# Optimization experiments

Measured on AMD Instinct MI355X. Metric: run time of the kernel, lower is better.

## Reference

```python
import jax, jax.numpy as jnp
import numpy as np

EPS = 1e-5
K = 9  # 3x3 kernel taps


def _deform_conv_bn_relu(x, w_off, b_off, w, gamma, beta):
    B, C, H, W = x.shape
    dt = x.dtype
    # offset-predicting conv: [B, 2*K, H, W], channel layout (y,x) pairs per tap (mmcv v1)
    offset = jax.lax.conv_general_dilated(
        x, w_off, window_strides=(1, 1), padding=((1, 1), (1, 1)),
        dimension_numbers=('NCHW', 'OIHW', 'NCHW')) + b_off[None, :, None, None]
    off = offset.reshape(B, K, 2, H, W)
    # kernel tap displacements relative to output pixel (padding=1 -> centered 3x3)
    dy = (jnp.arange(K) // 3 - 1).astype(dt)
    dx = (jnp.arange(K) % 3 - 1).astype(dt)
    ii = jnp.arange(H, dtype=dt)[:, None]
    jj = jnp.arange(W, dtype=dt)[None, :]
    py = ii[None, None] + dy[None, :, None, None] + off[:, :, 0]  # [B,K,H,W]
    px = jj[None, None] + dx[None, :, None, None] + off[:, :, 1]
    y0 = jnp.floor(py)
    x0 = jnp.floor(px)
    ly = py - y0
    lx = px - x0

    xf = x.reshape(B, C, H * W)

    def gather(yc, xc, wt):
        # bilinear corner gather with zero padding outside the image
        valid = (yc >= 0) & (yc < H) & (xc >= 0) & (xc < W)
        yi = jnp.clip(yc, 0, H - 1).astype(jnp.int32)
        xi = jnp.clip(xc, 0, W - 1).astype(jnp.int32)
        idx = (yi * W + xi).reshape(B, -1)              # [B, K*H*W]
        g = jax.vmap(lambda xb, ib: xb[:, ib])(xf, idx)  # [B, C, K*H*W]
        wm = (wt * valid.astype(dt)).reshape(B, 1, -1)
        return g * wm

    val = (gather(y0, x0, (1 - ly) * (1 - lx))
           + gather(y0, x0 + 1, (1 - ly) * lx)
           + gather(y0 + 1, x0, ly * (1 - lx))
           + gather(y0 + 1, x0 + 1, ly * lx))
    val = val.reshape(B, C, K, H, W)

    # deformable conv accumulation (no bias in mmcv DeformConv2d v1)
    O = w.shape[0]
    out = jnp.einsum('ock,bckhw->bohw', w.reshape(O, C, K), val)

    # BatchNorm (training-mode batch stats) + ReLU
    mean = out.mean(axis=(0, 2, 3))
    var = out.var(axis=(0, 2, 3))
    out = (out - mean[None, :, None, None]) * jax.lax.rsqrt(var + EPS)[None, :, None, None]
    out = out * gamma[None, :, None, None] + beta[None, :, None, None]
    return jax.nn.relu(out)


def setup_inputs() -> dict:
    key = jax.random.key(0)
    k1, k2, k3 = jax.random.split(key, 3)
    B, C, O, H, W = 2, 256, 256, 128, 128
    x = jax.random.normal(k1, (B, C, H, W), dtype=jnp.float32)
    # offset branch: small init so predicted offsets stay in a realistic range
    w_off = jax.random.normal(k2, (2 * K, C, 3, 3), dtype=jnp.float32) * 0.01
    b_off = jnp.zeros((2 * K,), dtype=jnp.float32)
    w = jax.random.normal(k3, (O, C, 3, 3), dtype=jnp.float32) * 0.05
    gamma = jnp.ones((O,), dtype=jnp.float32)
    beta = jnp.zeros((O,), dtype=jnp.float32)
    return {"x": x, "w_off": w_off, "b_off": b_off, "w": w, "gamma": gamma, "beta": beta}


def reference(x, w_off, b_off, w, gamma, beta):
    return _deform_conv_bn_relu(x, w_off, b_off, w, gamma, beta)
```

## Files before the change

### kernel.cpp

```cpp
#include <hip/hip_runtime.h>
#include <hip/hip_bf16.h>

#define HWs   16384
#define Wimg  128
#define Himg  128
#define PW    130
#define PHW   16900
#define Cin   256
#define Oout  256
#define CKd   2304
#define Bb    2

typedef short   bf16x8 __attribute__((ext_vector_type(8)));
typedef float   f32x4  __attribute__((ext_vector_type(4)));

__device__ __forceinline__ float bf2f(ushort u){
  union { unsigned int i; float f; } v; v.i = ((unsigned int)u) << 16; return v.f;
}
__device__ __forceinline__ ushort f2bf(float f){
  union { float f; unsigned int i; } v; v.f = f;
  return (ushort)((v.i + 0x8000u) >> 16);
}
__device__ __forceinline__ unsigned cvt_pk_bf16(float lo, float hi){
  unsigned r;
  asm("v_cvt_pk_bf16_f32 %0, %1, %2" : "=v"(r) : "v"(lo), "v"(hi));
  return r;
}
__device__ __forceinline__ void gload_lds16(const ushort* g, void* l){
  __builtin_amdgcn_global_load_lds(
      (const __attribute__((address_space(1))) unsigned int*)g,
      (__attribute__((address_space(3))) unsigned int*)l, 16, 0, 0);
}

__global__ __launch_bounds__(256) void k_transpose(const float* __restrict__ x,
                                                   ushort* __restrict__ xtp){
  int bx = blockIdx.x;
  int b  = bx >> 10;
  int r  = bx & 1023;
  int ct = r >> 8;
  int pt = r & 255;
  int c0 = ct * 64, p0 = pt * 64;
  __shared__ float tile[64][65];
  const float* xb = x + (size_t)b * Cin * HWs;
  #pragma unroll
  for (int pass = 0; pass < 16; ++pass){
    int idx = pass * 256 + threadIdx.x;
    int cl = idx >> 6, pl = idx & 63;
    tile[cl][pl] = xb[(size_t)(c0 + cl) * HWs + p0 + pl];
  }
  __syncthreads();
  ushort* xo = xtp + (size_t)b * PHW * Cin;
  #pragma unroll
  for (int pass = 0; pass < 16; ++pass){
    int idx = pass * 256 + threadIdx.x;
    int pl = idx >> 6, cl = idx & 63;
    int hw = p0 + pl; int y = hw >> 7, xc = hw & 127;
    xo[(size_t)((y + 1) * PW + xc + 1) * Cin + c0 + cl] = f2bf(tile[cl][pl]);
  }
}

__global__ __launch_bounds__(64) void k_border(ushort* __restrict__ xtp){
  int e = blockIdx.x;
  int b = e / 516, p = e % 516;
  int y, xc;
  if (p < 130)      { y = 0;       xc = p; }
  else if (p < 260) { y = 129;     xc = p - 130; }
  else if (p < 388) { y = p - 259; xc = 0; }
  else              { y = p - 387; xc = 129; }
  uint2* dst = (uint2*)(xtp + ((size_t)b * PHW + y * PW + xc) * Cin) + threadIdx.x;
  *dst = make_uint2(0u, 0u);
}

__global__ __launch_bounds__(256) void k_wprep(const float* __restrict__ w,
                                               const float* __restrict__ wof,
                                               ushort* __restrict__ w2,
                                               ushort* __restrict__ w2of){
  int idx = blockIdx.x * 256 + threadIdx.x;
  if (idx < Oout * CKd){
    int o = idx / CKd, r = idx % CKd;
    int k = r >> 8, c = r & 255;
    w2[idx] = f2bf(w[(size_t)(o * Cin + c) * 9 + k]);
  } else {
    int j = idx - Oout * CKd;
    int o = j / CKd, r = j % CKd;
    int k = r >> 8, c = r & 255;
    float v = (o < 18) ? wof[(size_t)(o * Cin + c) * 9 + k] : 0.f;
    w2of[j] = f2bf(v);
  }
}

__global__ __launch_bounds__(512, 4) void k_offconv(const ushort* __restrict__ xtp,
                                                    const ushort* __restrict__ w2of,
                                                    const float* __restrict__ b_off,
                                                    int4* __restrict__ pidx,
                                                    float4* __restrict__ pw){
  int bx = blockIdx.x;
  int blkm = ((bx & 7) << 6) | (bx >> 3);
  int b = blkm >> 8, tile = blkm & 255;
  int hw0 = tile * 64;
  int iy = tile >> 1, jx0 = (tile & 1) * 64;
  __shared__ __align__(16) ushort aw[2][2048];
  __shared__ __align__(16) ushort bv_s[2][4096];
  __shared__ float offs_lds[18][64];
  int t = threadIdx.x, lane = t & 63, wid = t >> 6;
  int mi = wid >> 2, ni = wid & 3;
  f32x4 acc = (f32x4){0,0,0,0};
  const ushort* xb = xtp + (size_t)b * PHW * Cin;

#define OSTAGE(S, P) \
  if ((S) < 36){ int kks = (S) * 64, kt = (S) >> 2, c0s = ((S) * 64) & 255; \
    int dy = kt / 3 - 1, dxx = kt % 3 - 1; \
    if (wid < 4){ int L = t * 16; int oo = L >> 7; int inb = (L & 127) ^ ((oo & 7) << 4); \
      gload_lds16(w2of + (size_t)oo * CKd + kks + (inb >> 1), (char*)aw[P] + L); } \
    { int L = t * 16; int hw_l = L >> 7; int inb = (L & 127) ^ ((hw_l & 7) << 4); \
      int row = (iy + dy + 1) * PW + (jx0 + hw_l + dxx + 1); \
      gload_lds16(xb + (size_t)row * Cin + c0s + (inb >> 1), (char*)bv_s[P] + L); } }

  OSTAGE(0, 0);
  __syncthreads();
  #pragma unroll 1
  for (int step = 0; step < 36; ++step){
    int P = step & 1;
    OSTAGE(step + 1, P ^ 1);
    #pragma unroll
    for (int kk2 = 0; kk2 < 2; ++kk2){
      int coff = kk2 * 64 + ((lane >> 4) << 4);
      bf16x8 a0, bb;
      { int r = mi * 16 + (lane & 15); int byte = r * 128 + coff; byte ^= ((r & 7) << 4); a0 = *(const bf16x8*)((char*)aw[P] + byte); }
      { int r = ni * 16 + (lane & 15); int byte = r * 128 + coff; byte ^= ((r & 7) << 4); bb = *(const bf16x8*)((char*)bv_s[P] + byte); }
      acc = __builtin_amdgcn_mfma_f32_16x16x32_bf16(a0, bb, acc, 0, 0, 0);
    }
    __syncthreads();
  }
#undef OSTAGE
  {
    int hw_l = ni * 16 + (lane & 15);
    #pragma unroll
    for (int r = 0; r < 4; ++r){
      int o = mi * 16 + ((lane >> 4) << 2) + r;
      if (o < 18) offs_lds[o][hw_l] = acc[r] + b_off[o];
    }
  }
  __syncthreads();
  for (int idx = t; idx < 9 * 64; idx += 512){
    int k = idx >> 6, jl = idx & 63;
    int hw = hw0 + jl;
    int i = hw >> 7, jcol = hw & 127;
    float offy = offs_lds[2 * k][jl];
    float offx = offs_lds[2 * k + 1][jl];
    float py = (float)i    + (float)(k / 3 - 1) + offy;
    float px = (float)jcol + (float)(k % 3 - 1) + offx;
    float y0f = floorf(py), x0f = floorf(px);
    float ly = py - y0f, lx = px - x0f;
    int y0 = (int)y0f, x0 = (int)x0f;
    int y1 = y0 + 1, x1 = x0 + 1;
    float w00 = (1.f - ly) * (1.f - lx), w01 = (1.f - ly) * lx;
    float w10 = ly * (1.f - lx),         w11 = ly * lx;
    bool vy0 = (y0 >= 0 && y0 < 128), vy1 = (y1 >= 0 && y1 < 128);
    bool vx0 = (x0 >= 0 && x0 < 128), vx1 = (x1 >= 0 && x1 < 128);
    int iy0 = min(max(y0, 0), 127), iy1 = min(max(y1, 0), 127);
    int ix0 = min(max(x0, 0), 127), ix1 = min(max(x1, 0), 127);
    size_t e = ((size_t)b * 9 + k) * HWs + hw;
    pidx[e] = make_int4(((iy0 + 1) * PW + ix0 + 1) * Cin, ((iy0 + 1) * PW + ix1 + 1) * Cin,
                        ((iy1 + 1) * PW + ix0 + 1) * Cin, ((iy1 + 1) * PW + ix1 + 1) * Cin);
    pw[e]   = make_float4(vy0 && vx0 ? w00 : 0.f, vy0 && vx1 ? w01 : 0.f,
                          vy1 && vx0 ? w10 : 0.f, vy1 && vx1 ? w11 : 0.f);
  }
}

__device__ __forceinline__ unsigned combine_pair(unsigned d0, unsigned d1, unsigned d2, unsigned d3,
                                                 float4 wt){
  float e0 = wt.x * __uint_as_float(d0 << 16)
           + wt.y * __uint_as_float(d1 << 16)
           + wt.z * __uint_as_float(d2 << 16)
           + wt.w * __uint_as_float(d3 << 16);
  float e1 = wt.x * __uint_as_float(d0 & 0xFFFF0000u)
           + wt.y * __uint_as_float(d1 & 0xFFFF0000u)
           + wt.z * __uint_as_float(d2 & 0xFFFF0000u)
           + wt.w * __uint_as_float(d3 & 0xFFFF0000u);
  return cvt_pk_bf16(e0, e1);
}

__global__ __launch_bounds__(512, 2) void k_main(const ushort* __restrict__ xtp,
                                                 const ushort* __restrict__ w2,
                                                 const int4* __restrict__ pidx,
                                                 const float4* __restrict__ pw,
                                                 float* __restrict__ out,
                                                 float* __restrict__ partials){
  int bx = blockIdx.x;
  int blkm = ((bx & 7) << 5) | (bx >> 3);
  int b = blkm >> 7, tile = blkm & 127;
  int hw0 = tile * 128;
  __shared__ __align__(16) ushort smem[49152];
  ushort* Ab0 = smem;
  ushort* Ab1 = smem + 16384;
  ushort* Bb0 = smem + 32768;
  ushort* Bb1 = smem + 40960;
  int t = threadIdx.x, lane = t & 63, wid = t >> 6;
  int wm = wid >> 1, wn = wid & 1;
  int cg = t & 7, hl = t >> 3;
  f32x4 acc[4][4];
  #pragma unroll
  for (int mi = 0; mi < 4; ++mi)
    #pragma unroll
    for (int ni = 0; ni < 4; ++ni) acc[mi][ni] = (f32x4){0,0,0,0};
  const ushort* xb  = xtp  + (size_t)b * PHW * Cin;
  const int4*   pib = pidx + (size_t)b * 9 * HWs + hw0;
  const float4* pwb = pw   + (size_t)b * 9 * HWs + hw0;

  int4   ids[2][2];
  float4 wts[2][2];
  uint4  g[2][2][4];

#define PIPE_BARRIER() do { \
    asm volatile("s_waitcnt vmcnt(12) lgkmcnt(0)" ::: "memory"); \
    __builtin_amdgcn_sched_barrier(0); \
    __builtin_amdgcn_s_barrier(); \
    __builtin_amdgcn_sched_barrier(0); \
  } while (0)

#define IDSLOAD(P, S) \
  { int kq = ((S) < 35 ? (S) : 35) >> 2; \
    ids[P][0] = pib[(size_t)kq * HWs + hl]; \
    ids[P][1] = pib[(size_t)kq * HWs + hl + 64]; }

#define CORNERS(P, S) \
  { int Sc = ((S) < 35 ? (S) : 35); \
    int cb = ((Sc * 64) & 255) + cg * 8; int kq = Sc >> 2; \
    wts[P][0] = pwb[(size_t)kq * HWs + hl]; \
    wts[P][1] = pwb[(size_t)kq * HWs + hl + 64]; \
    _Pragma("unroll") for (int hh = 0; hh < 2; ++hh){ \
      g[P][hh][0] = *(const uint4*)(xb + ids[P][hh].x + cb); \
      g[P][hh][1] = *(const uint4*)(xb + ids[P][hh].y + cb); \
      g[P][hh][2] = *(const uint4*)(xb + ids[P][hh].z + cb); \
      g[P][hh][3] = *(const uint4*)(xb + ids[P][hh].w + cb); } }

#define STAGEA(S, ABP) \
  { int kks = ((S) < 35 ? (S) : 35) * 64; \
    _Pragma("unroll") for (int h2 = 0; h2 < 4; ++h2){ \
      int L = (wid * 4 + h2) * 1024 + lane * 16; \
      int oo = L >> 7; int inb = (L & 127) ^ ((oo & 7) << 4); \
      gload_lds16(w2 + (size_t)oo * CKd + kks + (inb >> 1), (char*)(ABP) + L); } }

#define COMBINE(P, S, BBP) \
  { _Pragma("unroll") for (int hh = 0; hh < 2; ++hh){ \
      int hw_l = hl + hh * 64; \
      float4 wtv = wts[P][hh]; \
      uint4 ov; \
      ov.x = combine_pair(g[P][hh][0].x, g[P][hh][1].x, g[P][hh][2].x, g[P][hh][3].x, wtv); \
      ov.y = combine_pair(g[P][hh][0].y, g[P][hh][1].y, g[P][hh][2].y, g[P][hh][3].y, wtv); \
      ov.z = combine_pair(g[P][hh][0].z, g[P][hh][1].z, g[P][hh][2].z, g[P][hh][3].z, wtv); \
      ov.w = combine_pair(g[P][hh][0].w, g[P][hh][1].w, g[P][hh][2].w, g[P][hh][3].w, wtv); \
      int byte = hw_l * 128 + cg * 16; byte ^= ((hw_l & 7) << 4); \
      *(uint4*)((char*)(BBP) + byte) = ov; } }

#define MFMA_PHASE(ABP, BBP) \
  { __builtin_amdgcn_s_setprio(1); \
    _Pragma("unroll") for (int kk2 = 0; kk2 < 2; ++kk2){ \
      int coff = kk2 * 64 + ((lane >> 4) << 4); \
      bf16x8 a[4], bv[4]; \
      _Pragma("unroll") for (int mi = 0; mi < 4; ++mi){ \
        int r = wm * 64 + mi * 16 + (lane & 15); \
        int byte = r * 128 + coff; byte ^= ((r & 7) << 4); \
        a[mi] = *(const bf16x8*)((const char*)(ABP) + byte); } \
      _Pragma("unroll") for (int ni = 0; ni < 4; ++ni){ \
        int r = wn * 64 + ni * 16 + (lane & 15); \
        int byte = r * 128 + coff; byte ^= ((r & 7) << 4); \
        bv[ni] = *(const bf16x8*)((const char*)(BBP) + byte); } \
      _Pragma("unroll") for (int mi = 0; mi < 4; ++mi) \
        _Pragma("unroll") for (int ni = 0; ni < 4; ++ni) \
          acc[mi][ni] = __builtin_amdgcn_mfma_f32_16x16x32_bf16(a[mi], bv[ni], acc[mi][ni], 0, 0, 0); } \
    __builtin_amdgcn_s_setprio(0); }

  STAGEA(0, Ab0);
  IDSLOAD(0, 0);
  IDSLOAD(1, 1);
  CORNERS(0, 0);
  IDSLOAD(0, 2);
  CORNERS(1, 1);
  IDSLOAD(1, 3);
  COMBINE(0, 0, Bb0);
  PIPE_BARRIER();

  #pragma unroll 1
  for (int tt = 0; tt < 36; tt += 2){
    STAGEA(tt + 1, Ab1);
    CORNERS(0, tt + 2);
    IDSLOAD(0, tt + 4);
    MFMA_PHASE(Ab0, Bb0);
    COMBINE(1, tt + 1, Bb1);
    PIPE_BARRIER();
    STAGEA(tt + 2, Ab0);
    CORNERS(1, tt + 3);
    IDSLOAD(1, tt + 5);
    MFMA_PHASE(Ab1, Bb1);
    COMBINE(0, tt + 2, Bb0);
    PIPE_BARRIER();
  }
#undef PIPE_BARRIER
#undef IDSLOAD
#undef CORNERS
#undef STAGEA
#undef COMBINE
#undef MFMA_PHASE

  #pragma unroll
  for (int mi = 0; mi < 4; ++mi){
    int obase = wm * 64 + mi * 16 + ((lane >> 4) << 2);
    #pragma unroll
    for (int ni = 0; ni < 4; ++ni){
      int hw = hw0 + wn * 64 + ni * 16 + (lane & 15);
      float* op = out + ((size_t)b * Oout + obase) * HWs + hw;
      #pragma unroll
      for (int r = 0; r < 4; ++r) op[(size_t)r * HWs] = acc[mi][ni][r];
    }
  }
  #pragma unroll
  for (int mi = 0; mi < 4; ++mi){
    #pragma unroll
    for (int r = 0; r < 4; ++r){
      float s = 0.f, s2 = 0.f;
      #pragma unroll
      for (int ni = 0; ni < 4; ++ni){ float v = acc[mi][ni][r]; s += v; s2 += v * v; }
      #pragma unroll
      for (int off2 = 1; off2 < 16; off2 <<= 1){
        s  += __shfl_xor(s, off2);
        s2 += __shfl_xor(s2, off2);
      }
      if ((lane & 15) == 0){
        int o = wm * 64 + mi * 16 + ((lane >> 4) << 2) + r;
        int row = blkm * 2 + wn;
        partials[(size_t)row * 256 + o] = s;
        partials[(size_t)512 * 256 + (size_t)row * 256 + o] = s2;
      }
    }
  }
}

__global__ __launch_bounds__(256) void k_bnstats(const float* __restrict__ partials,
                                                 float* __restrict__ stats){
  int o = blockIdx.x, t = threadIdx.x;
  float s = 0.f, s2 = 0.f;
  for (int i = t; i < 512; i += 256){
    s  += partials[(size_t)i * 256 + o];
    s2 += partials[(size_t)512 * 256 + (size_t)i * 256 + o];
  }
  #pragma unroll
  for (int off = 32; off > 0; off >>= 1){
    s  += __shfl_down(s, off);
    s2 += __shfl_down(s2, off);
  }
  __shared__ float rs[4], rs2[4];
  int lane = t & 63, w = t >> 6;
  if (lane == 0){ rs[w] = s; rs2[w] = s2; }
  __syncthreads();
  if (t == 0){
    float S = 0.f, S2 = 0.f;
    for (int i = 0; i < 4; ++i){ S += rs[i]; S2 += rs2[i]; }
    float mean = S / 32768.f;
    float var  = S2 / 32768.f - mean * mean;
    stats[o] = mean;
    stats[256 + o] = rsqrtf(var + 1e-5f);
  }
}

__global__ __launch_bounds__(256) void k_bnapply(float* __restrict__ out,
                                                 const float* __restrict__ stats,
                                                 const float* __restrict__ gamma,
                                                 const float* __restrict__ beta){
  size_t e = ((size_t)blockIdx.x * 256 + threadIdx.x) * 4;
  int o = (int)((e >> 14) & 255);
  float mean = stats[o], rstd = stats[256 + o];
  float sc = rstd * gamma[o];
  float sh = beta[o] - mean * sc;
  float4 v = *(float4*)(out + e);
  v.x = fmaxf(v.x * sc + sh, 0.f);
  v.y = fmaxf(v.y * sc + sh, 0.f);
  v.z = fmaxf(v.z * sc + sh, 0.f);
  v.w = fmaxf(v.w * sc + sh, 0.f);
  *(float4*)(out + e) = v;
}

extern "C" void kernel_launch(void* const* d_in, const int* in_sizes, int n_in,
                              void* d_out, int out_size, void* d_ws, size_t ws_size,
                              hipStream_t stream){
  const float* x     = (const float*)d_in[0];
  const float* w_off = (const float*)d_in[1];
  const float* b_off = (const float*)d_in[2];
  const float* w     = (const float*)d_in[3];
  const float* gamma = (const float*)d_in[4];
  const float* beta  = (const float*)d_in[5];
  float* out = (float*)d_out;

  char* p = (char*)d_ws;
  ushort* xtp  = (ushort*)p; p += (size_t)Bb * PHW * Cin * 2;
  ushort* w2   = (ushort*)p; p += (size_t)Oout * CKd * 2;
  ushort* w2of = (ushort*)p; p += (size_t)32 * CKd * 2;
  int4*   pidx = (int4*)p;   p += (size_t)Bb * 9 * HWs * 16;
  float4* pwt  = (float4*)p; p += (size_t)Bb * 9 * HWs * 16;
  float*  parts= (float*)p;  p += (size_t)2 * 512 * 256 * 4;
  float*  stats= (float*)p;

  k_transpose<<<dim3(2048), dim3(256), 0, stream>>>(x, xtp);
  k_border   <<<dim3(1032), dim3(64),  0, stream>>>(xtp);
  k_wprep    <<<dim3(2592), dim3(256), 0, stream>>>(w, w_off, w2, w2of);
  k_offconv  <<<dim3(512),  dim3(512), 0, stream>>>(xtp, w2of, b_off, pidx, pwt);
  k_main     <<<dim3(256),  dim3(512), 0, stream>>>(xtp, w2, pidx, pwt, out, parts);
  k_bnstats  <<<dim3(256),  dim3(256), 0, stream>>>(parts, stats);
  k_bnapply  <<<dim3(8192), dim3(256), 0, stream>>>(out, stats, gamma, beta);
}
```

Measured before the change: 129.1 us.

## Load weight A-fragments directly from global into registers instead of LDS staging

The weight operand is no longer staged through shared memory with global_load_lds. Each wave now loads its MFMA A-fragments straight from global memory into registers, software-pipelined per K half-step. This halves LDS usage, which may allow more occupancy, and drops the LDS writes and reads for A. In exchange, weights are re-read from global/L2 by both wn waves, the vmcnt-based wait is removed, and the loads are uncoalesced strided fragment loads whose latency must be hidden by the MFMA work.

```diff
diff --git a/kernel.cpp b/kernel.cpp
--- a/kernel.cpp
+++ b/kernel.cpp
@@ -14,9 +14,6 @@
 typedef short   bf16x8 __attribute__((ext_vector_type(8)));
 typedef float   f32x4  __attribute__((ext_vector_type(4)));
 
-__device__ __forceinline__ float bf2f(ushort u){
-  union { unsigned int i; float f; } v; v.i = ((unsigned int)u) << 16; return v.f;
-}
 __device__ __forceinline__ ushort f2bf(float f){
   union { float f; unsigned int i; } v; v.f = f;
   return (ushort)((v.i + 0x8000u) >> 16);
@@ -191,11 +188,8 @@
   int blkm = ((bx & 7) << 5) | (bx >> 3);
   int b = blkm >> 7, tile = blkm & 127;
   int hw0 = tile * 128;
-  __shared__ __align__(16) ushort smem[49152];
-  ushort* Ab0 = smem;
-  ushort* Ab1 = smem + 16384;
-  ushort* Bb0 = smem + 32768;
-  ushort* Bb1 = smem + 40960;
+  __shared__ __align__(16) ushort Bb0[8192];
+  __shared__ __align__(16) ushort Bb1[8192];
   int t = threadIdx.x, lane = t & 63, wid = t >> 6;
   int wm = wid >> 1, wn = wid & 1;
   int cg = t & 7, hl = t >> 3;
@@ -207,25 +201,27 @@
   const ushort* xb  = xtp  + (size_t)b * PHW * Cin;
   const int4*   pib = pidx + (size_t)b * 9 * HWs + hw0;
   const float4* pwb = pw   + (size_t)b * 9 * HWs + hw0;
+  const ushort* w2t = w2 + (size_t)(wm * 64 + (lane & 15)) * CKd + ((lane >> 4) << 3);
 
   int4   ids[2][2];
   float4 wts[2][2];
   uint4  g[2][2][4];
+  bf16x8 a0[4], a1[4];
 
 #define PIPE_BARRIER() do { \
-    asm volatile("s_waitcnt vmcnt(12) lgkmcnt(0)" ::: "memory"); \
+    asm volatile("s_waitcnt lgkmcnt(0)" ::: "memory"); \
     __builtin_amdgcn_sched_barrier(0); \
     __builtin_amdgcn_s_barrier(); \
     __builtin_amdgcn_sched_barrier(0); \
   } while (0)
 
 #define IDSLOAD(P, S) \
-  { int kq = ((S) < 35 ? (S) : 35) >> 2; \
+  { int kq = ((S) < 36 ? (S) : 35) >> 2; \
     ids[P][0] = pib[(size_t)kq * HWs + hl]; \
     ids[P][1] = pib[(size_t)kq * HWs + hl + 64]; }
 
 #define CORNERS(P, S) \
-  { int Sc = ((S) < 35 ? (S) : 35); \
+  { int Sc = ((S) < 36 ? (S) : 35); \
     int cb = ((Sc * 64) & 255) + cg * 8; int kq = Sc >> 2; \
     wts[P][0] = pwb[(size_t)kq * HWs + hl]; \
     wts[P][1] = pwb[(size_t)kq * HWs + hl + 64]; \
@@ -235,12 +231,10 @@
       g[P][hh][2] = *(const uint4*)(xb + ids[P][hh].z + cb); \
       g[P][hh][3] = *(const uint4*)(xb + ids[P][hh].w + cb); } }
 
-#define STAGEA(S, ABP) \
-  { int kks = ((S) < 35 ? (S) : 35) * 64; \
-    _Pragma("unroll") for (int h2 = 0; h2 < 4; ++h2){ \
-      int L = (wid * 4 + h2) * 1024 + lane * 16; \
-      int oo = L >> 7; int inb = (L & 127) ^ ((oo & 7) << 4); \
-      gload_lds16(w2 + (size_t)oo * CKd + kks + (inb >> 1), (char*)(ABP) + L); } }
+#define ALOAD(A, S, KK2) \
+  { int kks = ((S) < 36 ? (S) : 35) * 64 + (KK2) * 32; \
+    _Pragma("unroll") for (int mi = 0; mi < 4; ++mi) \
+      A[mi] = *(const bf16x8*)(w2t + (size_t)mi * 16 * CKd + kks); }
 
 #define COMBINE(P, S, BBP) \
   { _Pragma("unroll") for (int hh = 0; hh < 2; ++hh){ \
@@ -254,55 +248,54 @@
       int byte = hw_l * 128 + cg * 16; byte ^= ((hw_l & 7) << 4); \
       *(uint4*)((char*)(BBP) + byte) = ov; } }
 
-#define MFMA_PHASE(ABP, BBP) \
-  { __builtin_amdgcn_s_setprio(1); \
-    _Pragma("unroll") for (int kk2 = 0; kk2 < 2; ++kk2){ \
-      int coff = kk2 * 64 + ((lane >> 4) << 4); \
-      bf16x8 a[4], bv[4]; \
-      _Pragma("unroll") for (int mi = 0; mi < 4; ++mi){ \
-        int r = wm * 64 + mi * 16 + (lane & 15); \
-        int byte = r * 128 + coff; byte ^= ((r & 7) << 4); \
-        a[mi] = *(const bf16x8*)((const char*)(ABP) + byte); } \
-      _Pragma("unroll") for (int ni = 0; ni < 4; ++ni){ \
-        int r = wn * 64 + ni * 16 + (lane & 15); \
-        int byte = r * 128 + coff; byte ^= ((r & 7) << 4); \
-        bv[ni] = *(const bf16x8*)((const char*)(BBP) + byte); } \
-      _Pragma("unroll") for (int mi = 0; mi < 4; ++mi) \
-        _Pragma("unroll") for (int ni = 0; ni < 4; ++ni) \
-          acc[mi][ni] = __builtin_amdgcn_mfma_f32_16x16x32_bf16(a[mi], bv[ni], acc[mi][ni], 0, 0, 0); } \
+#define MFMA_K(A, KK2, BBP) \
+  { int coff = (KK2) * 64 + ((lane >> 4) << 4); \
+    bf16x8 bv[4]; \
+    _Pragma("unroll") for (int ni = 0; ni < 4; ++ni){ \
+      int r = wn * 64 + ni * 16 + (lane & 15); \
+      int byte = r * 128 + coff; byte ^= ((r & 7) << 4); \
+      bv[ni] = *(const bf16x8*)((const char*)(BBP) + byte); } \
+    __builtin_amdgcn_s_setprio(1); \
+    _Pragma("unroll") for (int mi = 0; mi < 4; ++mi) \
+      _Pragma("unroll") for (int ni = 0; ni < 4; ++ni) \
+        acc[mi][ni] = __builtin_amdgcn_mfma_f32_16x16x32_bf16(A[mi], bv[ni], acc[mi][ni], 0, 0, 0); \
     __builtin_amdgcn_s_setprio(0); }
 
-  STAGEA(0, Ab0);
   IDSLOAD(0, 0);
   IDSLOAD(1, 1);
   CORNERS(0, 0);
   IDSLOAD(0, 2);
   CORNERS(1, 1);
   IDSLOAD(1, 3);
+  ALOAD(a0, 0, 0);
   COMBINE(0, 0, Bb0);
   PIPE_BARRIER();
 
   #pragma unroll 1
   for (int tt = 0; tt < 36; tt += 2){
-    STAGEA(tt + 1, Ab1);
+    ALOAD(a1, tt, 1);
     CORNERS(0, tt + 2);
     IDSLOAD(0, tt + 4);
-    MFMA_PHASE(Ab0, Bb0);
+    MFMA_K(a0, 0, Bb0);
+    ALOAD(a0, tt + 1, 0);
+    MFMA_K(a1, 1, Bb0);
     COMBINE(1, tt + 1, Bb1);
     PIPE_BARRIER();
-    STAGEA(tt + 2, Ab0);
+    ALOAD(a1, tt + 1, 1);
     CORNERS(1, tt + 3);
     IDSLOAD(1, tt + 5);
-    MFMA_PHASE(Ab1, Bb1);
+    MFMA_K(a0, 0, Bb1);
+    ALOAD(a0, tt + 2, 0);
+    MFMA_K(a1, 1, Bb1);
     COMBINE(0, tt + 2, Bb0);
     PIPE_BARRIER();
   }
 #undef PIPE_BARRIER
 #undef IDSLOAD
 #undef CORNERS
-#undef STAGEA
+#undef ALOAD
 #undef COMBINE
-#undef MFMA_PHASE
+#undef MFMA_K
 
   #pragma unroll
   for (int mi = 0; mi < 4; ++mi){
```

Measured after the change: 156.8 us. +21.5%, slower.
